# Kernel tuning notes

Measured on AMD Instinct MI355X. Metric: run time of the kernel, lower is better.

Reference implementation:

```python
import jax, jax.numpy as jnp
import numpy as np

VOCAB, EMBED, BLOCK, HEADS, LAYERS = 96, 192, 128, 6, 6
HS = EMBED // HEADS  # 32
B, T = 256, 128
EPS = 1e-5


def layer_norm(x, g, b):
    m = jnp.mean(x, axis=-1, keepdims=True)
    v = jnp.mean(jnp.square(x - m), axis=-1, keepdims=True)
    return (x - m) * jax.lax.rsqrt(v + EPS) * g + b


def setup_inputs() -> dict:
    key = jax.random.key(0)
    ks = jax.random.split(key, 20)
    s = 0.02
    return {
        "index": jax.random.randint(ks[0], (B, T), 0, VOCAB),
        "targets": jax.random.randint(ks[1], (B, T), 0, VOCAB),
        "tok_emb": jax.random.normal(ks[2], (VOCAB, EMBED), jnp.float32) * s,
        "pos_emb": jax.random.normal(ks[3], (BLOCK, EMBED), jnp.float32) * s,
        "ln1_g": jnp.ones((LAYERS, EMBED), jnp.float32),
        "ln1_b": jnp.zeros((LAYERS, EMBED), jnp.float32),
        "ln2_g": jnp.ones((LAYERS, EMBED), jnp.float32),
        "ln2_b": jnp.zeros((LAYERS, EMBED), jnp.float32),
        "Wq": jax.random.normal(ks[4], (LAYERS, HEADS, EMBED, HS), jnp.float32) * s,
        "Wk": jax.random.normal(ks[5], (LAYERS, HEADS, EMBED, HS), jnp.float32) * s,
        "Wv": jax.random.normal(ks[6], (LAYERS, HEADS, EMBED, HS), jnp.float32) * s,
        "W1": jax.random.normal(ks[7], (LAYERS, EMBED, 4 * EMBED), jnp.float32) * s,
        "b1": jnp.zeros((LAYERS, 4 * EMBED), jnp.float32),
        "W2": jax.random.normal(ks[8], (LAYERS, 4 * EMBED, EMBED), jnp.float32) * s,
        "b2": jnp.zeros((LAYERS, EMBED), jnp.float32),
        "fn_g": jnp.ones((EMBED,), jnp.float32),
        "fn_b": jnp.zeros((EMBED,), jnp.float32),
        "Wf": jax.random.normal(ks[9], (EMBED, VOCAB), jnp.float32) * s,
        "bf": jnp.zeros((VOCAB,), jnp.float32),
    }


def reference(index, targets, tok_emb, pos_emb, ln1_g, ln1_b, ln2_g, ln2_b,
              Wq, Wk, Wv, W1, b1, W2, b2, fn_g, fn_b, Wf, bf):
    t = index.shape[1]
    x = tok_emb[index] + pos_emb[:t]                      # [B,T,E]
    causal = jnp.tril(jnp.ones((t, t), bool))             # [T,T]
    for l in range(LAYERS):
        n1 = layer_norm(x, ln1_g[l], ln1_b[l])
        # --- per-head attention, computed but (faithfully) unused by the block ---
        q = jnp.einsum('bte,hes->bhts', n1, Wq[l])
        k = jnp.einsum('bte,hes->bhts', n1, Wk[l])
        v = jnp.einsum('bte,hes->bhts', n1, Wv[l])
        w = jnp.einsum('bhts,bhus->bhtu', q, k) * (EMBED ** -0.5)  # note: scaled by embed, as in source
        w = jnp.where(causal, w, -jnp.inf)
        wei = jax.nn.softmax(w, axis=-1)
        _attn_out = jnp.einsum('bhtu,bhus->bhts', wei, v)  # dead in original forward
        # --- actual block output: FFN on ln2(ln1(x)), no residual ---
        n2 = layer_norm(n1, ln2_g[l], ln2_b[l])
        h = jnp.maximum(jnp.einsum('bte,ef->btf', n2, W1[l]) + b1[l], 0.0)
        x = jnp.einsum('btf,fe->bte', h, W2[l]) + b2[l]
    x = layer_norm(x, fn_g, fn_b)
    logits = jnp.einsum('bte,ev->btv', x, Wf) + bf        # [B,T,V]
    pred = logits.reshape(-1, VOCAB)                      # [B*T,V]
    tgt = targets.reshape(-1)
    logp = jax.nn.log_softmax(pred, axis=-1)
    loss = -jnp.mean(jnp.take_along_axis(logp, tgt[:, None], axis=1)[:, 0])
    return pred, loss
```

## Files before the change

kernel.cpp:

```cpp
#include <hip/hip_runtime.h>

typedef __attribute__((ext_vector_type(4))) float f32x4;
typedef __attribute__((ext_vector_type(8))) short short8;
typedef unsigned short ushort_t;
typedef unsigned int uint_t;

#define R_  32768
#define L_  6
#define EPS_ 1e-5f

#define NW_ 884736

__device__ __forceinline__ ushort_t f2bf(float f) {
    uint_t i = __builtin_bit_cast(uint_t, f);
    uint_t r = (i + 0x7fffu + ((i >> 16) & 1u)) >> 16;
    return (ushort_t)r;
}
__device__ __forceinline__ uint_t cvtpk(float a, float b) {
    uint_t r;
    asm("v_cvt_pk_bf16_f32 %0, %1, %2" : "=v"(r) : "v"(a), "v"(b));
    return r;
}

__global__ void wconv_k(const float* __restrict__ W1, const float* __restrict__ W2,
                        const float* __restrict__ Wf,
                        ushort_t* __restrict__ w1s, ushort_t* __restrict__ w2s,
                        ushort_t* __restrict__ wfr)
{
    int i = blockIdx.x * 256 + threadIdx.x;
    if (i < NW_) {
        int j = i & 7, li = (i >> 3) & 63, q = i >> 9;
        int kc = q % 6; q /= 6;
        int ft = q % 6; q /= 6;
        int wv = q & 3; q >>= 2;
        int half = q & 1; int l = q >> 1;
        int f = half * 384 + wv * 96 + ft * 16 + (li & 15);
        int k = kc * 32 + ((li >> 4) << 3) + j;
        w1s[i] = f2bf(W1[((size_t)l * 192 + k) * 768 + f]);
        return;
    }
    i -= NW_;
    if (i < NW_) {
        int j = i & 7, li = (i >> 3) & 63, q = i >> 9;
        int kc2 = q % 12; q /= 12;
        int ei = q % 3; q /= 3;
        int wv = q & 3; q >>= 2;
        int half = q & 1; int l = q >> 1;
        int e = (wv + 4 * ei) * 16 + (li & 15);
        int k = half * 384 + kc2 * 32 + ((li >> 4) << 3) + j;
        w2s[i] = f2bf(W2[((size_t)l * 768 + k) * 192 + e]);
        return;
    }
    i -= NW_;
    if (i < 36 * 512) {
        int j = i & 7, li = (i >> 3) & 63, q = i >> 9;
        int kc = q % 6, vt = q / 6;
        int v = vt * 16 + (li & 15);
        int k = kc * 32 + ((li >> 4) << 3) + j;
        wfr[i] = f2bf(Wf[(size_t)k * 96 + v]);
    }
}

__global__ __launch_bounds__(256, 2) void net_k(
    const int* __restrict__ idxp, const int* __restrict__ tgp,
    const float* __restrict__ tok, const float* __restrict__ pos,
    const float* __restrict__ ln1g, const float* __restrict__ ln1b,
    const float* __restrict__ ln2g, const float* __restrict__ ln2b,
    const float* __restrict__ b1g, const float* __restrict__ b2g,
    const float* __restrict__ fng, const float* __restrict__ fnb,
    const float* __restrict__ bfb,
    const ushort_t* __restrict__ w1s, const ushort_t* __restrict__ w2s,
    const ushort_t* __restrict__ wfr,
    float* __restrict__ pred, float* __restrict__ partial)
{
    __shared__ __align__(16) ushort_t xb[6 * 4 * 512];
    __shared__ __align__(16) ushort_t hbl[12 * 4 * 512];
    __shared__ __align__(16) float lnS1[64][4], lnQ1[64][4];
    __shared__ __align__(16) float lnS2[64][4], lnQ2[64][4];
    __shared__ float lsred[4];

    const int tid = threadIdx.x, lane = tid & 63, w = tid >> 6;
    const int c = lane & 15, g = lane >> 4;
    const int row0 = blockIdx.x * 64;

    f32x4 xac[3][4];

#pragma unroll
    for (int rg = 0; rg < 4; ++rg) {
        int row = row0 + rg * 16 + c;
        int id = idxp[row];
        int tt = row & 127;
#pragma unroll
        for (int i = 0; i < 3; ++i) {
            int e0 = (w + 4 * i) * 16 + g * 4;
            float4 a = *(const float4*)(tok + (size_t)id * 192 + e0);
            float4 b = *(const float4*)(pos + (size_t)tt * 192 + e0);
            xac[i][rg][0] = a.x + b.x; xac[i][rg][1] = a.y + b.y;
            xac[i][rg][2] = a.z + b.z; xac[i][rg][3] = a.w + b.w;
        }
    }

#pragma unroll 1
    for (int l = 0; l < L_; ++l) {
#pragma unroll
        for (int rg = 0; rg < 4; ++rg) {
            float s = 0.f, sq = 0.f;
#pragma unroll
            for (int i = 0; i < 3; ++i)
#pragma unroll
                for (int r = 0; r < 4; ++r) { float v = xac[i][rg][r]; s += v; sq += v * v; }
            s += __shfl_xor(s, 16); sq += __shfl_xor(sq, 16);
            s += __shfl_xor(s, 32); sq += __shfl_xor(sq, 32);
            if (g == 0) { lnS1[rg * 16 + c][w] = s; lnQ1[rg * 16 + c][w] = sq; }
        }
        __syncthreads();
#pragma unroll
        for (int rg = 0; rg < 4; ++rg) {
            float4 S = *(const float4*)lnS1[rg * 16 + c];
            float4 Q = *(const float4*)lnQ1[rg * 16 + c];
            float mu = (S.x + S.y + S.z + S.w) * (1.f / 192.f);
            float var = (Q.x + Q.y + Q.z + Q.w) * (1.f / 192.f) - mu * mu;
            float ri = rsqrtf(var + EPS_);
            float s2 = 0.f, q2 = 0.f;
#pragma unroll
            for (int i = 0; i < 3; ++i) {
                int e0 = (w + 4 * i) * 16 + g * 4;
                float4 gg = *(const float4*)(ln1g + l * 192 + e0);
                float4 bb = *(const float4*)(ln1b + l * 192 + e0);
                float n0 = (xac[i][rg][0] - mu) * ri * gg.x + bb.x;
                float n1 = (xac[i][rg][1] - mu) * ri * gg.y + bb.y;
                float n2 = (xac[i][rg][2] - mu) * ri * gg.z + bb.z;
                float n3 = (xac[i][rg][3] - mu) * ri * gg.w + bb.w;
                xac[i][rg][0] = n0; xac[i][rg][1] = n1; xac[i][rg][2] = n2; xac[i][rg][3] = n3;
                s2 += n0 + n1 + n2 + n3;
                q2 += n0 * n0 + n1 * n1 + n2 * n2 + n3 * n3;
            }
            s2 += __shfl_xor(s2, 16); q2 += __shfl_xor(q2, 16);
            s2 += __shfl_xor(s2, 32); q2 += __shfl_xor(q2, 32);
            if (g == 0) { lnS2[rg * 16 + c][w] = s2; lnQ2[rg * 16 + c][w] = q2; }
        }
        __syncthreads();
#pragma unroll
        for (int rg = 0; rg < 4; ++rg) {
            float4 S = *(const float4*)lnS2[rg * 16 + c];
            float4 Q = *(const float4*)lnQ2[rg * 16 + c];
            float mu = (S.x + S.y + S.z + S.w) * (1.f / 192.f);
            float var = (Q.x + Q.y + Q.z + Q.w) * (1.f / 192.f) - mu * mu;
            float ri = rsqrtf(var + EPS_);
#pragma unroll
            for (int i = 0; i < 3; ++i) {
                int et = w + 4 * i;
                int e0 = et * 16 + g * 4;
                float4 gg = *(const float4*)(ln2g + l * 192 + e0);
                float4 bb = *(const float4*)(ln2b + l * 192 + e0);
                float y0 = (xac[i][rg][0] - mu) * ri * gg.x + bb.x;
                float y1 = (xac[i][rg][1] - mu) * ri * gg.y + bb.y;
                float y2 = (xac[i][rg][2] - mu) * ri * gg.z + bb.z;
                float y3 = (xac[i][rg][3] - mu) * ri * gg.w + bb.w;
                uint_t d0 = cvtpk(y0, y1), d1 = cvtpk(y2, y3);
                int kc = et >> 1, floc = ((et & 1) << 4) + g * 4;
                int us = (kc * 4 + rg) * 512 + ((floc >> 3) * 16 + c) * 8 + (floc & 7);
                *(uint2*)(xb + us) = make_uint2(d0, d1);
                xac[i][rg][0] = 0.f; xac[i][rg][1] = 0.f; xac[i][rg][2] = 0.f; xac[i][rg][3] = 0.f;
            }
        }
        __syncthreads();

#pragma unroll 1
        for (int half = 0; half < 2; ++half) {
            const ushort_t* w1p = w1s + ((size_t)((l * 2 + half) * 4 + w) * 36) * 512 + lane * 8;
#pragma unroll
            for (int fth = 0; fth < 2; ++fth) {
                short8 wa[18];
#pragma unroll
                for (int q = 0; q < 18; ++q) wa[q] = *(const short8*)(w1p + (fth * 18 + q) * 512);
                float4 bbv[3];
#pragma unroll
                for (int f3 = 0; f3 < 3; ++f3)
                    bbv[f3] = *(const float4*)(b1g + l * 768 + half * 384 + w * 96 + (fth * 3 + f3) * 16 + g * 4);
#pragma unroll
                for (int rg = 0; rg < 4; ++rg) {
                    short8 xbf[6];
#pragma unroll
                    for (int kc = 0; kc < 6; ++kc)
                        xbf[kc] = *(const short8*)(xb + (kc * 4 + rg) * 512 + lane * 8);
#pragma unroll
                    for (int f3 = 0; f3 < 3; ++f3) {
                        f32x4 acc = {};
                        __builtin_amdgcn_s_setprio(1);
#pragma unroll
                        for (int kc = 0; kc < 6; ++kc)
                            acc = __builtin_amdgcn_mfma_f32_16x16x32_bf16(wa[f3 * 6 + kc], xbf[kc], acc, 0, 0, 0);
                        __builtin_amdgcn_s_setprio(0);
                        float y0 = fmaxf(acc[0] + bbv[f3].x, 0.f);
                        float y1 = fmaxf(acc[1] + bbv[f3].y, 0.f);
                        float y2 = fmaxf(acc[2] + bbv[f3].z, 0.f);
                        float y3 = fmaxf(acc[3] + bbv[f3].w, 0.f);
                        uint_t d0 = cvtpk(y0, y1), d1 = cvtpk(y2, y3);
                        int ft = fth * 3 + f3;
                        int kc2 = w * 3 + (ft >> 1);
                        int floc = ((ft & 1) << 4) + g * 4;
                        int us = (kc2 * 4 + rg) * 512 + ((floc >> 3) * 16 + c) * 8 + (floc & 7);
                        *(uint2*)(hbl + us) = make_uint2(d0, d1);
                    }
                }
            }
            __syncthreads();

            const ushort_t* w2p = w2s + ((size_t)((l * 2 + half) * 4 + w) * 36) * 512 + lane * 8;
#pragma unroll
            for (int kh = 0; kh < 2; ++kh) {
                short8 wr[18];
#pragma unroll
                for (int ei = 0; ei < 3; ++ei)
#pragma unroll
                    for (int k6 = 0; k6 < 6; ++k6)
                        wr[ei * 6 + k6] = *(const short8*)(w2p + (ei * 12 + kh * 6 + k6) * 512);
#pragma unroll
                for (int rg = 0; rg < 4; ++rg) {
                    short8 hbf[6];
#pragma unroll
                    for (int k6 = 0; k6 < 6; ++k6)
                        hbf[k6] = *(const short8*)(hbl + ((kh * 6 + k6) * 4 + rg) * 512 + lane * 8);
                    __builtin_amdgcn_s_setprio(1);
#pragma unroll
                    for (int ei = 0; ei < 3; ++ei)
#pragma unroll
                        for (int k6 = 0; k6 < 6; ++k6)
                            xac[ei][rg] = __builtin_amdgcn_mfma_f32_16x16x32_bf16(wr[ei * 6 + k6], hbf[k6], xac[ei][rg], 0, 0, 0);
                    __builtin_amdgcn_s_setprio(0);
                }
            }
            __syncthreads();
        }

#pragma unroll
        for (int i = 0; i < 3; ++i) {
            int e0 = (w + 4 * i) * 16 + g * 4;
            float4 bb = *(const float4*)(b2g + l * 192 + e0);
#pragma unroll
            for (int rg = 0; rg < 4; ++rg) {
                xac[i][rg][0] += bb.x; xac[i][rg][1] += bb.y;
                xac[i][rg][2] += bb.z; xac[i][rg][3] += bb.w;
            }
        }
    }

#pragma unroll
    for (int rg = 0; rg < 4; ++rg) {
        float s = 0.f, sq = 0.f;
#pragma unroll
        for (int i = 0; i < 3; ++i)
#pragma unroll
            for (int r = 0; r < 4; ++r) { float v = xac[i][rg][r]; s += v; sq += v * v; }
        s += __shfl_xor(s, 16); sq += __shfl_xor(sq, 16);
        s += __shfl_xor(s, 32); sq += __shfl_xor(sq, 32);
        if (g == 0) { lnS1[rg * 16 + c][w] = s; lnQ1[rg * 16 + c][w] = sq; }
    }
    __syncthreads();
#pragma unroll
    for (int rg = 0; rg < 4; ++rg) {
        float4 S = *(const float4*)lnS1[rg * 16 + c];
        float4 Q = *(const float4*)lnQ1[rg * 16 + c];
        float mu = (S.x + S.y + S.z + S.w) * (1.f / 192.f);
        float var = (Q.x + Q.y + Q.z + Q.w) * (1.f / 192.f) - mu * mu;
        float ri = rsqrtf(var + EPS_);
#pragma unroll
        for (int i = 0; i < 3; ++i) {
            int et = w + 4 * i;
            int e0 = et * 16 + g * 4;
            float4 gg = *(const float4*)(fng + e0);
            float4 bb = *(const float4*)(fnb + e0);
            float y0 = (xac[i][rg][0] - mu) * ri * gg.x + bb.x;
            float y1 = (xac[i][rg][1] - mu) * ri * gg.y + bb.y;
            float y2 = (xac[i][rg][2] - mu) * ri * gg.z + bb.z;
            float y3 = (xac[i][rg][3] - mu) * ri * gg.w + bb.w;
            uint_t d0 = cvtpk(y0, y1), d1 = cvtpk(y2, y3);
            int kc = et >> 1, floc = ((et & 1) << 4) + g * 4;
            int us = (kc * 4 + rg) * 512 + ((floc >> 3) * 16 + c) * 8 + (floc & 7);
            *(uint2*)(xb + us) = make_uint2(d0, d1);
        }
    }
    __syncthreads();

    short8 wfh[36];
    {
        const ushort_t* wfp = wfr + lane * 8;
#pragma unroll
        for (int q = 0; q < 36; ++q) wfh[q] = *(const short8*)(wfp + q * 512);
    }
    short8 xbf[6];
#pragma unroll
    for (int kc = 0; kc < 6; ++kc)
        xbf[kc] = *(const short8*)(xb + (kc * 4 + w) * 512 + lane * 8);
    f32x4 av[6] = {};
    __builtin_amdgcn_s_setprio(1);
#pragma unroll
    for (int vt = 0; vt < 6; ++vt)
#pragma unroll
        for (int kc = 0; kc < 6; ++kc)
            av[vt] = __builtin_amdgcn_mfma_f32_16x16x32_bf16(wfh[vt * 6 + kc], xbf[kc], av[vt], 0, 0, 0);
    __builtin_amdgcn_s_setprio(0);

    float vv[6][4];
#pragma unroll
    for (int vt = 0; vt < 6; ++vt) {
        float4 bb = *(const float4*)(bfb + vt * 16 + g * 4);
        vv[vt][0] = av[vt][0] + bb.x;
        vv[vt][1] = av[vt][1] + bb.y;
        vv[vt][2] = av[vt][2] + bb.z;
        vv[vt][3] = av[vt][3] + bb.w;
    }
    float mx = -1e30f;
#pragma unroll
    for (int vt = 0; vt < 6; ++vt)
#pragma unroll
        for (int r = 0; r < 4; ++r) mx = fmaxf(mx, vv[vt][r]);
    mx = fmaxf(mx, __shfl_xor(mx, 16));
    mx = fmaxf(mx, __shfl_xor(mx, 32));
    float se = 0.f;
#pragma unroll
    for (int vt = 0; vt < 6; ++vt)
#pragma unroll
        for (int r = 0; r < 4; ++r) se += expf(vv[vt][r] - mx);
    se += __shfl_xor(se, 16);
    se += __shfl_xor(se, 32);
    float lse = logf(se) + mx;
    int myrow = row0 + w * 16 + c;
    int tgt = tgp[myrow];
    float lsum = 0.f;
#pragma unroll
    for (int vt = 0; vt < 6; ++vt)
#pragma unroll
        for (int r = 0; r < 4; ++r)
            if (tgt == vt * 16 + g * 4 + r) lsum += lse - vv[vt][r];
#pragma unroll
    for (int vt = 0; vt < 6; ++vt) {
        float4 o;
        o.x = vv[vt][0]; o.y = vv[vt][1]; o.z = vv[vt][2]; o.w = vv[vt][3];
        *(float4*)(pred + (size_t)myrow * 96 + vt * 16 + g * 4) = o;
    }
#pragma unroll
    for (int m = 1; m < 64; m <<= 1) lsum += __shfl_xor(lsum, m);
    if (lane == 0) lsred[w] = lsum;
    __syncthreads();
    if (tid == 0) partial[blockIdx.x] = lsred[0] + lsred[1] + lsred[2] + lsred[3];
}

__global__ void lossred_k(const float* __restrict__ partial, float* __restrict__ out)
{
    __shared__ double sd[256];
    int t = threadIdx.x;
    sd[t] = (double)partial[t] + (double)partial[t + 256];
    __syncthreads();
    for (int s = 128; s > 0; s >>= 1) {
        if (t < s) sd[t] += sd[t + s];
        __syncthreads();
    }
    if (t == 0) out[0] = (float)(sd[0] / (double)R_);
}

extern "C" void kernel_launch(void* const* d_in, const int* in_sizes, int n_in,
                              void* d_out, int out_size, void* d_ws, size_t ws_size,
                              hipStream_t stream)
{
    (void)in_sizes; (void)n_in; (void)out_size; (void)ws_size;
    const int*   index   = (const int*)  d_in[0];
    const int*   targets = (const int*)  d_in[1];
    const float* tok     = (const float*)d_in[2];
    const float* pos     = (const float*)d_in[3];
    const float* ln1g    = (const float*)d_in[4];
    const float* ln1b    = (const float*)d_in[5];
    const float* ln2g    = (const float*)d_in[6];
    const float* ln2b    = (const float*)d_in[7];
    const float* W1      = (const float*)d_in[11];
    const float* b1      = (const float*)d_in[12];
    const float* W2      = (const float*)d_in[13];
    const float* b2      = (const float*)d_in[14];
    const float* fng     = (const float*)d_in[15];
    const float* fnb     = (const float*)d_in[16];
    const float* Wf      = (const float*)d_in[17];
    const float* bfv     = (const float*)d_in[18];

    ushort_t* w1s = (ushort_t*)d_ws;
    ushort_t* w2s = w1s + NW_;
    ushort_t* wfr = w2s + NW_;
    float* partial = (float*)(wfr + 36 * 512);
    float* pred  = (float*)d_out;
    float* lossp = pred + (size_t)R_ * 96;

    const int nconv = 2 * NW_ + 36 * 512;
    wconv_k<<<nconv / 256, 256, 0, stream>>>(W1, W2, Wf, w1s, w2s, wfr);
    net_k<<<512, 256, 0, stream>>>(index, targets, tok, pos, ln1g, ln1b, ln2g, ln2b,
                                   b1, b2, fng, fnb, bfv, w1s, w2s, wfr, pred, partial);
    lossred_k<<<1, 256, 0, stream>>>(partial, lossp);
}
```

Baseline: 149.9 us.

## Fuse double layernorm into single-pass stats and hoist activation fragments in FFN1

Computes the second layernorm's mean and variance algebraically from the first pass's moments (sums of x, x², g·x, g²x, (gx)², b·gx) together with per-layer gamma/beta reductions precomputed in the weight-conversion kernel. This removes one block-wide reduction and __syncthreads per layer. It also loads all 24 activation fragments once per half in the first FFN matmul and loops over 6 weight tiles of 6 chunks instead of 2 of 18, which changes register pressure. The moment expansion may lose precision compared with a direct variance computation.

```diff
diff --git a/kernel.cpp b/kernel.cpp
--- a/kernel.cpp
+++ b/kernel.cpp
@@ -24,8 +24,9 @@
 
 __global__ void wconv_k(const float* __restrict__ W1, const float* __restrict__ W2,
                         const float* __restrict__ Wf,
+                        const float* __restrict__ g1v, const float* __restrict__ b1v,
                         ushort_t* __restrict__ w1s, ushort_t* __restrict__ w2s,
-                        ushort_t* __restrict__ wfr)
+                        ushort_t* __restrict__ wfr, float* __restrict__ pc)
 {
     int i = blockIdx.x * 256 + threadIdx.x;
     if (i < NW_) {
@@ -58,6 +59,27 @@
         int v = vt * 16 + (li & 15);
         int k = kc * 32 + ((li >> 4) << 3) + j;
         wfr[i] = f2bf(Wf[(size_t)k * 96 + v]);
+        return;
+    }
+    i -= 36 * 512;
+    if (i < L_ * 64) {
+        int l = i >> 6, lane = i & 63;
+        float s = 0.f, s2 = 0.f, sgb = 0.f, sb = 0.f, sb2 = 0.f;
+#pragma unroll
+        for (int j = 0; j < 3; ++j) {
+            int e = lane * 3 + j;
+            float gg = g1v[l * 192 + e], bb = b1v[l * 192 + e];
+            s += gg; s2 += gg * gg; sgb += gg * bb; sb += bb; sb2 += bb * bb;
+        }
+#pragma unroll
+        for (int m = 1; m < 64; m <<= 1) {
+            s += __shfl_xor(s, m); s2 += __shfl_xor(s2, m);
+            sgb += __shfl_xor(sgb, m); sb += __shfl_xor(sb, m); sb2 += __shfl_xor(sb2, m);
+        }
+        if (lane == 0) {
+            pc[l * 8 + 0] = s;  pc[l * 8 + 1] = s2; pc[l * 8 + 2] = sgb;
+            pc[l * 8 + 3] = sb; pc[l * 8 + 4] = sb2;
+        }
     }
 }
 
@@ -70,13 +92,12 @@
     const float* __restrict__ fng, const float* __restrict__ fnb,
     const float* __restrict__ bfb,
     const ushort_t* __restrict__ w1s, const ushort_t* __restrict__ w2s,
-    const ushort_t* __restrict__ wfr,
+    const ushort_t* __restrict__ wfr, const float* __restrict__ pc,
     float* __restrict__ pred, float* __restrict__ partial)
 {
     __shared__ __align__(16) ushort_t xb[6 * 4 * 512];
     __shared__ __align__(16) ushort_t hbl[12 * 4 * 512];
-    __shared__ __align__(16) float lnS1[64][4], lnQ1[64][4];
-    __shared__ __align__(16) float lnS2[64][4], lnQ2[64][4];
+    __shared__ __align__(16) float lnB[64][28];
     __shared__ float lsred[4];
 
     const int tid = threadIdx.x, lane = tid & 63, w = tid >> 6;
@@ -102,107 +123,123 @@
 
 #pragma unroll 1
     for (int l = 0; l < L_; ++l) {
+        const float sg  = pc[l * 8 + 0], sg2 = pc[l * 8 + 1], sgb = pc[l * 8 + 2];
+        const float sb  = pc[l * 8 + 3], sb2 = pc[l * 8 + 4];
 #pragma unroll
         for (int rg = 0; rg < 4; ++rg) {
-            float s = 0.f, sq = 0.f;
-#pragma unroll
-            for (int i = 0; i < 3; ++i)
-#pragma unroll
-                for (int r = 0; r < 4; ++r) { float v = xac[i][rg][r]; s += v; sq += v * v; }
-            s += __shfl_xor(s, 16); sq += __shfl_xor(sq, 16);
-            s += __shfl_xor(s, 32); sq += __shfl_xor(sq, 32);
-            if (g == 0) { lnS1[rg * 16 + c][w] = s; lnQ1[rg * 16 + c][w] = sq; }
-        }
-        __syncthreads();
-#pragma unroll
-        for (int rg = 0; rg < 4; ++rg) {
-            float4 S = *(const float4*)lnS1[rg * 16 + c];
-            float4 Q = *(const float4*)lnQ1[rg * 16 + c];
-            float mu = (S.x + S.y + S.z + S.w) * (1.f / 192.f);
-            float var = (Q.x + Q.y + Q.z + Q.w) * (1.f / 192.f) - mu * mu;
-            float ri = rsqrtf(var + EPS_);
-            float s2 = 0.f, q2 = 0.f;
+            float S = 0.f, Q = 0.f, A = 0.f, A2 = 0.f, B2 = 0.f, C = 0.f;
 #pragma unroll
             for (int i = 0; i < 3; ++i) {
                 int e0 = (w + 4 * i) * 16 + g * 4;
-                float4 gg = *(const float4*)(ln1g + l * 192 + e0);
-                float4 bb = *(const float4*)(ln1b + l * 192 + e0);
-                float n0 = (xac[i][rg][0] - mu) * ri * gg.x + bb.x;
-                float n1 = (xac[i][rg][1] - mu) * ri * gg.y + bb.y;
-                float n2 = (xac[i][rg][2] - mu) * ri * gg.z + bb.z;
-                float n3 = (xac[i][rg][3] - mu) * ri * gg.w + bb.w;
-                xac[i][rg][0] = n0; xac[i][rg][1] = n1; xac[i][rg][2] = n2; xac[i][rg][3] = n3;
-                s2 += n0 + n1 + n2 + n3;
-                q2 += n0 * n0 + n1 * n1 + n2 * n2 + n3 * n3;
-            }
-            s2 += __shfl_xor(s2, 16); q2 += __shfl_xor(q2, 16);
-            s2 += __shfl_xor(s2, 32); q2 += __shfl_xor(q2, 32);
-            if (g == 0) { lnS2[rg * 16 + c][w] = s2; lnQ2[rg * 16 + c][w] = q2; }
+                float4 g1f = *(const float4*)(ln1g + l * 192 + e0);
+                float4 b1f = *(const float4*)(ln1b + l * 192 + e0);
+                float ga[4] = {g1f.x, g1f.y, g1f.z, g1f.w};
+                float ba[4] = {b1f.x, b1f.y, b1f.z, b1f.w};
+#pragma unroll
+                for (int r = 0; r < 4; ++r) {
+                    float x = xac[i][rg][r];
+                    float gx = ga[r] * x;
+                    S += x; Q = fmaf(x, x, Q); A += gx;
+                    A2 = fmaf(ga[r], gx, A2); B2 = fmaf(gx, gx, B2); C = fmaf(ba[r], gx, C);
+                }
+            }
+            S += __shfl_xor(S, 16);  S += __shfl_xor(S, 32);
+            Q += __shfl_xor(Q, 16);  Q += __shfl_xor(Q, 32);
+            A += __shfl_xor(A, 16);  A += __shfl_xor(A, 32);
+            A2 += __shfl_xor(A2, 16); A2 += __shfl_xor(A2, 32);
+            B2 += __shfl_xor(B2, 16); B2 += __shfl_xor(B2, 32);
+            C += __shfl_xor(C, 16);  C += __shfl_xor(C, 32);
+            if (g == 0) {
+                int row = rg * 16 + c;
+                lnB[row][0 * 4 + w] = S;  lnB[row][1 * 4 + w] = Q;  lnB[row][2 * 4 + w] = A;
+                lnB[row][3 * 4 + w] = A2; lnB[row][4 * 4 + w] = B2; lnB[row][5 * 4 + w] = C;
+            }
         }
         __syncthreads();
 #pragma unroll
         for (int rg = 0; rg < 4; ++rg) {
-            float4 S = *(const float4*)lnS2[rg * 16 + c];
-            float4 Q = *(const float4*)lnQ2[rg * 16 + c];
-            float mu = (S.x + S.y + S.z + S.w) * (1.f / 192.f);
-            float var = (Q.x + Q.y + Q.z + Q.w) * (1.f / 192.f) - mu * mu;
-            float ri = rsqrtf(var + EPS_);
+            int row = rg * 16 + c;
+            float4 S4 = *(const float4*)&lnB[row][0];
+            float4 Q4 = *(const float4*)&lnB[row][4];
+            float4 A4 = *(const float4*)&lnB[row][8];
+            float4 A24 = *(const float4*)&lnB[row][12];
+            float4 B24 = *(const float4*)&lnB[row][16];
+            float4 C4 = *(const float4*)&lnB[row][20];
+            float S = S4.x + S4.y + S4.z + S4.w;
+            float Q = Q4.x + Q4.y + Q4.z + Q4.w;
+            float A = A4.x + A4.y + A4.z + A4.w;
+            float A2 = A24.x + A24.y + A24.z + A24.w;
+            float B2 = B24.x + B24.y + B24.z + B24.w;
+            float C = C4.x + C4.y + C4.z + C4.w;
+            float mu1 = S * (1.f / 192.f);
+            float ri1 = rsqrtf(Q * (1.f / 192.f) - mu1 * mu1 + EPS_);
+            float Sy  = ri1 * (A - mu1 * sg) + sb;
+            float Sy2 = ri1 * ri1 * (B2 - 2.f * mu1 * A2 + mu1 * mu1 * sg2)
+                      + 2.f * ri1 * (C - mu1 * sgb) + sb2;
+            float mu2 = Sy * (1.f / 192.f);
+            float ri2 = rsqrtf(Sy2 * (1.f / 192.f) - mu2 * mu2 + EPS_);
+            float rr = ri1 * ri2;
 #pragma unroll
             for (int i = 0; i < 3; ++i) {
                 int et = w + 4 * i;
                 int e0 = et * 16 + g * 4;
-                float4 gg = *(const float4*)(ln2g + l * 192 + e0);
-                float4 bb = *(const float4*)(ln2b + l * 192 + e0);
-                float y0 = (xac[i][rg][0] - mu) * ri * gg.x + bb.x;
-                float y1 = (xac[i][rg][1] - mu) * ri * gg.y + bb.y;
-                float y2 = (xac[i][rg][2] - mu) * ri * gg.z + bb.z;
-                float y3 = (xac[i][rg][3] - mu) * ri * gg.w + bb.w;
-                uint_t d0 = cvtpk(y0, y1), d1 = cvtpk(y2, y3);
+                float4 g1f = *(const float4*)(ln1g + l * 192 + e0);
+                float4 b1f = *(const float4*)(ln1b + l * 192 + e0);
+                float4 g2f = *(const float4*)(ln2g + l * 192 + e0);
+                float4 b2f = *(const float4*)(ln2b + l * 192 + e0);
+                float ga[4] = {g1f.x, g1f.y, g1f.z, g1f.w};
+                float ba[4] = {b1f.x, b1f.y, b1f.z, b1f.w};
+                float gc[4] = {g2f.x, g2f.y, g2f.z, g2f.w};
+                float bc[4] = {b2f.x, b2f.y, b2f.z, b2f.w};
+                float y[4];
+#pragma unroll
+                for (int r = 0; r < 4; ++r) {
+                    float ca = ga[r] * gc[r] * rr;
+                    float u  = gc[r] * ri2;
+                    float cb = fmaf(u, ba[r] - mu2, bc[r]) - ca * mu1;
+                    y[r] = fmaf(ca, xac[i][rg][r], cb);
+                    xac[i][rg][r] = 0.f;
+                }
+                uint_t d0 = cvtpk(y[0], y[1]), d1 = cvtpk(y[2], y[3]);
                 int kc = et >> 1, floc = ((et & 1) << 4) + g * 4;
                 int us = (kc * 4 + rg) * 512 + ((floc >> 3) * 16 + c) * 8 + (floc & 7);
                 *(uint2*)(xb + us) = make_uint2(d0, d1);
-                xac[i][rg][0] = 0.f; xac[i][rg][1] = 0.f; xac[i][rg][2] = 0.f; xac[i][rg][3] = 0.f;
             }
         }
         __syncthreads();
 
 #pragma unroll 1
         for (int half = 0; half < 2; ++half) {
+            short8 xall[24];
+#pragma unroll
+            for (int q = 0; q < 24; ++q)
+                xall[q] = *(const short8*)(xb + q * 512 + lane * 8);
+
             const ushort_t* w1p = w1s + ((size_t)((l * 2 + half) * 4 + w) * 36) * 512 + lane * 8;
 #pragma unroll
-            for (int fth = 0; fth < 2; ++fth) {
-                short8 wa[18];
-#pragma unroll
-                for (int q = 0; q < 18; ++q) wa[q] = *(const short8*)(w1p + (fth * 18 + q) * 512);
-                float4 bbv[3];
-#pragma unroll
-                for (int f3 = 0; f3 < 3; ++f3)
-                    bbv[f3] = *(const float4*)(b1g + l * 768 + half * 384 + w * 96 + (fth * 3 + f3) * 16 + g * 4);
+            for (int ft = 0; ft < 6; ++ft) {
+                short8 wa6[6];
+#pragma unroll
+                for (int kc = 0; kc < 6; ++kc)
+                    wa6[kc] = *(const short8*)(w1p + (ft * 6 + kc) * 512);
+                float4 bbv = *(const float4*)(b1g + l * 768 + half * 384 + w * 96 + ft * 16 + g * 4);
 #pragma unroll
                 for (int rg = 0; rg < 4; ++rg) {
-                    short8 xbf[6];
+                    f32x4 acc = {};
+                    __builtin_amdgcn_s_setprio(1);
 #pragma unroll
                     for (int kc = 0; kc < 6; ++kc)
-                        xbf[kc] = *(const short8*)(xb + (kc * 4 + rg) * 512 + lane * 8);
-#pragma unroll
-                    for (int f3 = 0; f3 < 3; ++f3) {
-                        f32x4 acc = {};
-                        __builtin_amdgcn_s_setprio(1);
-#pragma unroll
-                        for (int kc = 0; kc < 6; ++kc)
-                            acc = __builtin_amdgcn_mfma_f32_16x16x32_bf16(wa[f3 * 6 + kc], xbf[kc], acc, 0, 0, 0);
-                        __builtin_amdgcn_s_setprio(0);
-                        float y0 = fmaxf(acc[0] + bbv[f3].x, 0.f);
-                        float y1 = fmaxf(acc[1] + bbv[f3].y, 0.f);
-                        float y2 = fmaxf(acc[2] + bbv[f3].z, 0.f);
-                        float y3 = fmaxf(acc[3] + bbv[f3].w, 0.f);
-                        uint_t d0 = cvtpk(y0, y1), d1 = cvtpk(y2, y3);
-                        int ft = fth * 3 + f3;
-                        int kc2 = w * 3 + (ft >> 1);
-                        int floc = ((ft & 1) << 4) + g * 4;
-                        int us = (kc2 * 4 + rg) * 512 + ((floc >> 3) * 16 + c) * 8 + (floc & 7);
-                        *(uint2*)(hbl + us) = make_uint2(d0, d1);
-                    }
+                        acc = __builtin_amdgcn_mfma_f32_16x16x32_bf16(wa6[kc], xall[kc * 4 + rg], acc, 0, 0, 0);
+                    __builtin_amdgcn_s_setprio(0);
+                    float y0 = fmaxf(acc[0] + bbv.x, 0.f);
+                    float y1 = fmaxf(acc[1] + bbv.y, 0.f);
+                    float y2 = fmaxf(acc[2] + bbv.z, 0.f);
+                    float y3 = fmaxf(acc[3] + bbv.w, 0.f);
+                    uint_t d0 = cvtpk(y0, y1), d1 = cvtpk(y2, y3);
+                    int kc2 = w * 3 + (ft >> 1);
+                    int floc = ((ft & 1) << 4) + g * 4;
+                    int us = (kc2 * 4 + rg) * 512 + ((floc >> 3) * 16 + c) * 8 + (floc & 7);
+                    *(uint2*)(hbl + us) = make_uint2(d0, d1);
                 }
             }
             __syncthreads();
@@ -255,13 +292,14 @@
             for (int r = 0; r < 4; ++r) { float v = xac[i][rg][r]; s += v; sq += v * v; }
         s += __shfl_xor(s, 16); sq += __shfl_xor(sq, 16);
         s += __shfl_xor(s, 32); sq += __shfl_xor(sq, 32);
-        if (g == 0) { lnS1[rg * 16 + c][w] = s; lnQ1[rg * 16 + c][w] = sq; }
+        if (g == 0) { lnB[rg * 16 + c][0 * 4 + w] = s; lnB[rg * 16 + c][1 * 4 + w] = sq; }
     }
     __syncthreads();
 #pragma unroll
     for (int rg = 0; rg < 4; ++rg) {
-        float4 S = *(const float4*)lnS1[rg * 16 + c];
-        float4 Q = *(const float4*)lnQ1[rg * 16 + c];
+        int row = rg * 16 + c;
+        float4 S = *(const float4*)&lnB[row][0];
+        float4 Q = *(const float4*)&lnB[row][4];
         float mu = (S.x + S.y + S.z + S.w) * (1.f / 192.f);
         float var = (Q.x + Q.y + Q.z + Q.w) * (1.f / 192.f) - mu * mu;
         float ri = rsqrtf(var + EPS_);
@@ -386,12 +424,14 @@
     ushort_t* w2s = w1s + NW_;
     ushort_t* wfr = w2s + NW_;
     float* partial = (float*)(wfr + 36 * 512);
+    float* pc = partial + 512;
     float* pred  = (float*)d_out;
     float* lossp = pred + (size_t)R_ * 96;
 
-    const int nconv = 2 * NW_ + 36 * 512;
-    wconv_k<<<nconv / 256, 256, 0, stream>>>(W1, W2, Wf, w1s, w2s, wfr);
+    const int nconv = 2 * NW_ + 36 * 512 + 512;
+    wconv_k<<<(nconv + 255) / 256, 256, 0, stream>>>(W1, W2, Wf, ln1g, ln1b,
+                                                     w1s, w2s, wfr, pc);
     net_k<<<512, 256, 0, stream>>>(index, targets, tok, pos, ln1g, ln1b, ln2g, ln2b,
-                                   b1, b2, fng, fnb, bfv, w1s, w2s, wfr, pred, partial);
+                                   b1, b2, fng, fnb, bfv, w1s, w2s, wfr, pc, pred, partial);
     lossred_k<<<1, 256, 0, stream>>>(partial, lossp);
 }
```

Measured after the change: 153.8 us. 2.6% more time.
